# Kernel optimization log

Measured on AMD Instinct MI355X. Metric: run time of the kernel, lower is better.

## Reference

```python
import jax, jax.numpy as jnp
import numpy as np
from functools import partial

H = 51  # hidden size hard-coded in the module


def _lstm_cell(x, h, c, W_ih, b_ih, W_hh, b_hh):
    # PyTorch LSTMCell gate order: i, f, g, o stacked along dim 0 of W (4H rows)
    gates = x @ W_ih.T + b_ih + h @ W_hh.T + b_hh  # [B, 4H]
    i, f, g, o = jnp.split(gates, 4, axis=-1)
    i = jax.nn.sigmoid(i)
    f = jax.nn.sigmoid(f)
    g = jnp.tanh(g)
    o = jax.nn.sigmoid(o)
    c_new = f * c + i * g
    h_new = o * jnp.tanh(c_new)
    return h_new, c_new


def setup_inputs() -> dict:
    key = jax.random.key(0)
    ks = jax.random.split(key, 11)
    B, T = 2048, 512
    bound = 1.0 / np.sqrt(H)  # torch LSTMCell/Linear default init: U(-1/sqrt(H), 1/sqrt(H))
    u = lambda k, shape: jax.random.uniform(k, shape, jnp.float32, -bound, bound)
    return {
        "x": jax.random.normal(ks[0], (B, T), dtype=jnp.float32),
        "future": 0,
        "W_ih1": u(ks[1], (4 * H, 1)),
        "b_ih1": u(ks[2], (4 * H,)),
        "W_hh1": u(ks[3], (4 * H, H)),
        "b_hh1": u(ks[4], (4 * H,)),
        "W_ih2": u(ks[5], (4 * H, H)),
        "b_ih2": u(ks[6], (4 * H,)),
        "W_hh2": u(ks[7], (4 * H, H)),
        "b_hh2": u(ks[8], (4 * H,)),
        "fc_w": u(ks[9], (1, H)),
        "fc_b": u(ks[10], (1,)),
    }


def reference(x, future, W_ih1, b_ih1, W_hh1, b_hh1,
              W_ih2, b_ih2, W_hh2, b_hh2, fc_w, fc_b):
    B = x.shape[0]
    z = jnp.zeros((B, H), dtype=x.dtype)

    def cell_stack(x_t, carry):
        h1, c1, h2, c2 = carry
        h1, c1 = _lstm_cell(x_t, h1, c1, W_ih1, b_ih1, W_hh1, b_hh1)
        h2, c2 = _lstm_cell(h1, h2, c2, W_ih2, b_ih2, W_hh2, b_hh2)
        out = h2 @ fc_w.T + fc_b  # [B, 1]
        return (h1, c1, h2, c2), out

    def step(carry, x_t):
        return cell_stack(x_t, carry)

    xs = jnp.swapaxes(x, 0, 1)[:, :, None]  # [T, B, 1]
    carry, outs = jax.lax.scan(step, (z, z, z, z), xs)  # outs: [T, B, 1]
    outputs = jnp.swapaxes(outs[:, :, 0], 0, 1)  # [B, T]

    if future > 0:
        last = outs[-1]  # [B, 1]

        def fstep(c, _):
            inner, out = c
            inner, out = cell_stack(out, inner)
            return (inner, out), out

        _, fouts = jax.lax.scan(fstep, (carry, last), None, length=future)
        outputs = jnp.concatenate([outputs, jnp.swapaxes(fouts[:, :, 0], 0, 1)], axis=1)

    return outputs
```

## Files before the change

### kernel.cpp

```cpp
#include <hip/hip_runtime.h>

#define HID   51
#define T_LEN 512
#define BT    8
#define NTH   832

#define X_OFF   0
#define OUT_OFF 4128
#define H1_OFF  8256
#define H2_OFF  9280

typedef _Float16 h8 __attribute__((ext_vector_type(8)));
typedef float    f4 __attribute__((ext_vector_type(4)));

__device__ __forceinline__ float fast_rcp(float x) { return __builtin_amdgcn_rcpf(x); }
__device__ __forceinline__ float sigm(float x) { return fast_rcp(1.0f + __expf(-x)); }
__device__ __forceinline__ float tanh_f(float x) {
    x = fminf(15.0f, fmaxf(-15.0f, x));
    float e = __expf(2.0f * x);
    return (e - 1.0f) * fast_rcp(e + 1.0f);
}
__device__ __forceinline__ float tanh_nc(float x) {
    float e = __expf(2.0f * x);
    return (e - 1.0f) * fast_rcp(e + 1.0f);
}

__device__ __forceinline__ float dpp_ror8(float v) {
    int t = __builtin_amdgcn_update_dpp(0, __float_as_int(v), 0x128, 0xf, 0xf, true);
    return __int_as_float(t);
}

__device__ __forceinline__ h8 cvt_frag1(const float* p) {
    float4 a = *(const float4*)p;
    float4 b = *(const float4*)(p + 4);
    h8 h;
    h[0] = (_Float16)a.x; h[1] = (_Float16)a.y; h[2] = (_Float16)a.z; h[3] = (_Float16)a.w;
    h[4] = (_Float16)b.x; h[5] = (_Float16)b.y; h[6] = (_Float16)b.z; h[7] = (_Float16)b.w;
    return h;
}

__device__ __forceinline__ float gate_update(const float G[4], float& c) {
    float iv = sigm(G[0]), fv = sigm(G[1]), gv = tanh_nc(G[2]), ov = sigm(G[3]);
    c = fv * c + iv * gv;
    return ov * tanh_f(c);
}

#define MFMA16(A, B, C) __builtin_amdgcn_mfma_f32_16x16x32_f16((A), (B), (C), 0, 0, 0)

__global__ __launch_bounds__(NTH)
void lstm_seq_kernel(const float* __restrict__ x,
                     const float* __restrict__ W_ih1, const float* __restrict__ b_ih1,
                     const float* __restrict__ W_hh1, const float* __restrict__ b_hh1,
                     const float* __restrict__ W_ih2, const float* __restrict__ b_ih2,
                     const float* __restrict__ W_hh2, const float* __restrict__ b_hh2,
                     const float* __restrict__ fc_w,  const float* __restrict__ fc_b,
                     float* __restrict__ out)
{
    __shared__ __align__(16) float sb[13312];

    const int tid   = threadIdx.x;
    const int b0    = blockIdx.x * BT;
    const int w     = tid >> 6;
    const int lane  = tid & 63;
    const int row16 = lane & 15;
    const int q4    = lane >> 4;
    const int col   = row16;

    h8 a1f[2];
    h8 a2f[4];

    for (int i = tid; i < 208 * 64; i += NTH) {
        int rp = i >> 6, k = i & 63;
        int j = rp >> 2, g = rp & 3;
        float v = 0.0f;
        if (j < HID) {
            if (k < HID)       v = W_hh1[(g * HID + j) * HID + k];
            else if (k == HID) v = W_ih1[g * HID + j];
        }
        sb[i] = v;
    }
    __syncthreads();
    #pragma unroll
    for (int kt = 0; kt < 2; ++kt)
        a1f[kt] = cvt_frag1(sb + (w * 16 + row16) * 64 + kt * 32 + q4 * 8);
    __syncthreads();

    for (int i = tid; i < 208 * 64; i += NTH) {
        int rp = i >> 6, k = i & 63;
        int j = rp >> 2, g = rp & 3;
        sb[i] = (j < HID && k < HID) ? W_ih2[(g * HID + j) * HID + k] : 0.0f;
    }
    __syncthreads();
    #pragma unroll
    for (int kt = 0; kt < 2; ++kt)
        a2f[kt] = cvt_frag1(sb + (w * 16 + row16) * 64 + kt * 32 + q4 * 8);
    __syncthreads();

    for (int i = tid; i < 208 * 64; i += NTH) {
        int rp = i >> 6, k = i & 63;
        int j = rp >> 2, g = rp & 3;
        float v = 0.0f;
        if (k < HID) {
            if (j < HID)        v = W_hh2[(g * HID + j) * HID + k];
            else if (rp == 204) v = fc_w[k];
        }
        sb[i] = v;
    }
    __syncthreads();
    #pragma unroll
    for (int kt = 0; kt < 2; ++kt)
        a2f[kt + 2] = cvt_frag1(sb + (w * 16 + row16) * 64 + kt * 32 + q4 * 8);
    __syncthreads();

    const int jq = 4 * w + q4;
    f4 bi1, bi2;
    #pragma unroll
    for (int g = 0; g < 4; ++g) {
        bi1[g] = (jq < HID) ? (b_ih1[g * HID + jq] + b_hh1[g * HID + jq]) : 0.f;
        bi2[g] = (jq < HID) ? (b_ih2[g * HID + jq] + b_hh2[g * HID + jq]) : 0.f;
    }
    const bool lay1 = (col < 8);
    const int  bsel = col & 7;
    const bool val  = (jq < HID);
    const int offh  = (lay1 ? H1_OFF : H2_OFF) * 2
                    + (jq >> 5) * 512 + ((((jq & 31) >> 3) << 4) + bsel) * 8 + (jq & 7);
    const bool xw = (jq == HID) && lay1;

    float* xl   = sb + X_OFF;
    float* outl = sb + OUT_OFF;
    for (int i = tid; i < BT * 516; i += NTH) {
        int b = i / 516, t = i - 516 * b;
        xl[i] = (t < T_LEN) ? x[(size_t)(b0 + b) * T_LEN + t] : 0.0f;
    }
    for (int i = tid; i < 2048; i += NTH) sb[H1_OFF + i] = 0.0f;

    float c = 0.f;
    const float fcb = fc_b[0];
    const bool outlane = (w == 12) && (q4 == 3) && (col < 8);
    const float* xq  = xl + bsel * 516;
    const float* rA0 = sb + H1_OFF + lane * 4;
    const float* rB0 = sb + H2_OFF + lane * 4;
    _Float16* hwp = (_Float16*)sb + offh;
    __syncthreads();

    if (lay1) {
        if (val) {
            float xv = xq[0];
            float G[4];
            #pragma unroll
            for (int g = 0; g < 4; ++g)
                G[g] = bi1[g] + W_ih1[g * HID + jq] * xv;
            float hv = gate_update(G, c);
            hwp[0] = (_Float16)hv;
        } else if (xw) {
            hwp[0] = (_Float16)xq[1];
        }
    }
    __syncthreads();

    auto body = [&](int i, int p) {
        const float* rA = rA0 + p * 512;
        const float* rB = rB0 + p * 512;
        h8 bh0 = *(const h8*)(rA);       h8 bh1 = *(const h8*)(rA + 256);
        h8 ch2 = *(const h8*)(rB);       h8 ch3 = *(const h8*)(rB + 256);

        if (xw) hwp[(p ^ 1) * 1024] = (_Float16)xq[i + 2];

        f4 s = bi1;
        s = MFMA16(a1f[0], bh0, s);
        s = MFMA16(a1f[1], bh1, s);
        f4 u = bi2;
        u = MFMA16(a2f[0], bh0, u);
        u = MFMA16(a2f[1], bh1, u);
        u = MFMA16(a2f[2], ch2, u);
        u = MFMA16(a2f[3], ch3, u);

        float fcv = u[0];
        float G[4];
        #pragma unroll
        for (int g = 0; g < 4; ++g) {
            float ur = dpp_ror8(u[g]);
            G[g] = lay1 ? s[g] : ur;
        }
        float hv = gate_update(G, c);
        if (val) hwp[(p ^ 1) * 1024] = (_Float16)hv;
        if (outlane && i >= 1) outl[col * 516 + (i - 1)] = fcb + fcv;
        __syncthreads();
    };
    for (int i = 0; i < T_LEN; i += 2) {
        body(i, 0);
        body(i + 1, 1);
    }
    body(T_LEN, 0);

    for (int i = tid; i < BT * T_LEN; i += NTH) {
        int b = i >> 9, tt = i & (T_LEN - 1);
        out[(size_t)(b0 + b) * T_LEN + tt] = outl[b * 516 + tt];
    }
}

extern "C" void kernel_launch(void* const* d_in, const int* in_sizes, int n_in,
                              void* d_out, int out_size, void* d_ws, size_t ws_size,
                              hipStream_t stream) {
    const float* x      = (const float*)d_in[0];
    const float* W_ih1  = (const float*)d_in[2];
    const float* b_ih1v = (const float*)d_in[3];
    const float* W_hh1  = (const float*)d_in[4];
    const float* b_hh1v = (const float*)d_in[5];
    const float* W_ih2  = (const float*)d_in[6];
    const float* b_ih2v = (const float*)d_in[7];
    const float* W_hh2  = (const float*)d_in[8];
    const float* b_hh2v = (const float*)d_in[9];
    const float* fc_w   = (const float*)d_in[10];
    const float* fc_b   = (const float*)d_in[11];
    float* out = (float*)d_out;

    dim3 grid(2048 / BT);
    dim3 block(NTH);
    lstm_seq_kernel<<<grid, block, 0, stream>>>(x, W_ih1, b_ih1v, W_hh1, b_hh1v,
                                                W_ih2, b_ih2v, W_hh2, b_hh2v,
                                                fc_w, fc_b, out);
}
```

Measured before the change: 376.6 us.

## Fold log2e scaling and biases into weights and split MFMA accumulation chain

Gate weights are pre-scaled by log2(e), or 2*log2(e) for the tanh gate, so the activations can call exp2 directly. Bias sums move into an extra weight column that multiplies a constant fp16 1.0 written into the hidden-state buffer, which removes the per-step bias accumulator setup. The second-layer MFMA chain is split into two independent accumulations that are summed at the end, shortening the serial dependency on each recurrent step. The trade-offs are that biases are now rounded to fp16 and the tanh clamp is gone, relying on the rcp formulation staying stable at extreme inputs.

```diff
diff --git a/kernel.cpp b/kernel.cpp
--- a/kernel.cpp
+++ b/kernel.cpp
@@ -10,19 +10,22 @@
 #define H1_OFF  8256
 #define H2_OFF  9280
 
+#define L2E 1.4426950408889634f
+
 typedef _Float16 h8 __attribute__((ext_vector_type(8)));
 typedef float    f4 __attribute__((ext_vector_type(4)));
 
 __device__ __forceinline__ float fast_rcp(float x) { return __builtin_amdgcn_rcpf(x); }
-__device__ __forceinline__ float sigm(float x) { return fast_rcp(1.0f + __expf(-x)); }
-__device__ __forceinline__ float tanh_f(float x) {
-    x = fminf(15.0f, fmaxf(-15.0f, x));
-    float e = __expf(2.0f * x);
-    return (e - 1.0f) * fast_rcp(e + 1.0f);
-}
-__device__ __forceinline__ float tanh_nc(float x) {
-    float e = __expf(2.0f * x);
-    return (e - 1.0f) * fast_rcp(e + 1.0f);
+
+#if __has_builtin(__builtin_amdgcn_exp2f)
+__device__ __forceinline__ float exp2_f(float x) { return __builtin_amdgcn_exp2f(x); }
+#else
+__device__ __forceinline__ float exp2_f(float x) { return exp2f(x); }
+#endif
+
+__device__ __forceinline__ float sigm2(float X) { return fast_rcp(1.0f + exp2_f(-X)); }
+__device__ __forceinline__ float tanh2(float E) {
+    return fmaf(-2.0f, fast_rcp(exp2_f(E) + 1.0f), 1.0f);
 }
 
 __device__ __forceinline__ float dpp_ror8(float v) {
@@ -40,9 +43,12 @@
 }
 
 __device__ __forceinline__ float gate_update(const float G[4], float& c) {
-    float iv = sigm(G[0]), fv = sigm(G[1]), gv = tanh_nc(G[2]), ov = sigm(G[3]);
-    c = fv * c + iv * gv;
-    return ov * tanh_f(c);
+    float iv = sigm2(G[0]);
+    float fv = sigm2(G[1]);
+    float gv = tanh2(G[2]);
+    float ov = sigm2(G[3]);
+    c = fmaf(fv, c, iv * gv);
+    return ov * tanh2(c * (2.0f * L2E));
 }
 
 #define MFMA16(A, B, C) __builtin_amdgcn_mfma_f32_16x16x32_f16((A), (B), (C), 0, 0, 0)
@@ -72,10 +78,12 @@
     for (int i = tid; i < 208 * 64; i += NTH) {
         int rp = i >> 6, k = i & 63;
         int j = rp >> 2, g = rp & 3;
+        float sc = (g == 2) ? 2.0f * L2E : L2E;
         float v = 0.0f;
         if (j < HID) {
-            if (k < HID)       v = W_hh1[(g * HID + j) * HID + k];
-            else if (k == HID) v = W_ih1[g * HID + j];
+            if (k < HID)           v = W_hh1[(g * HID + j) * HID + k] * sc;
+            else if (k == HID)     v = W_ih1[g * HID + j] * sc;
+            else if (k == HID + 1) v = (b_ih1[g * HID + j] + b_hh1[g * HID + j]) * sc;
         }
         sb[i] = v;
     }
@@ -88,7 +96,13 @@
     for (int i = tid; i < 208 * 64; i += NTH) {
         int rp = i >> 6, k = i & 63;
         int j = rp >> 2, g = rp & 3;
-        sb[i] = (j < HID && k < HID) ? W_ih2[(g * HID + j) * HID + k] : 0.0f;
+        float sc = (g == 2) ? 2.0f * L2E : L2E;
+        float v = 0.0f;
+        if (j < HID) {
+            if (k < HID)           v = W_ih2[(g * HID + j) * HID + k] * sc;
+            else if (k == HID + 1) v = (b_ih2[g * HID + j] + b_hh2[g * HID + j]) * sc;
+        }
+        sb[i] = v;
     }
     __syncthreads();
     #pragma unroll
@@ -99,9 +113,10 @@
     for (int i = tid; i < 208 * 64; i += NTH) {
         int rp = i >> 6, k = i & 63;
         int j = rp >> 2, g = rp & 3;
+        float sc = (g == 2) ? 2.0f * L2E : L2E;
         float v = 0.0f;
         if (k < HID) {
-            if (j < HID)        v = W_hh2[(g * HID + j) * HID + k];
+            if (j < HID)        v = W_hh2[(g * HID + j) * HID + k] * sc;
             else if (rp == 204) v = fc_w[k];
         }
         sb[i] = v;
@@ -113,12 +128,6 @@
     __syncthreads();
 
     const int jq = 4 * w + q4;
-    f4 bi1, bi2;
-    #pragma unroll
-    for (int g = 0; g < 4; ++g) {
-        bi1[g] = (jq < HID) ? (b_ih1[g * HID + jq] + b_hh1[g * HID + jq]) : 0.f;
-        bi2[g] = (jq < HID) ? (b_ih2[g * HID + jq] + b_hh2[g * HID + jq]) : 0.f;
-    }
     const bool lay1 = (col < 8);
     const int  bsel = col & 7;
     const bool val  = (jq < HID);
@@ -132,7 +141,15 @@
         int b = i / 516, t = i - 516 * b;
         xl[i] = (t < T_LEN) ? x[(size_t)(b0 + b) * T_LEN + t] : 0.0f;
     }
-    for (int i = tid; i < 2048; i += NTH) sb[H1_OFF + i] = 0.0f;
+    for (int i = tid; i < 2048; i += NTH) {
+        int w32 = 0;
+        if (i < 1024) {
+            int r = i & 511;
+            int d = r - 386;
+            if (d >= 0 && d < 32 && (d & 3) == 0) w32 = 0x00003C00;
+        }
+        ((int*)(sb + H1_OFF))[i] = w32;
+    }
 
     float c = 0.f;
     const float fcb = fc_b[0];
@@ -141,6 +158,7 @@
     const float* rA0 = sb + H1_OFF + lane * 4;
     const float* rB0 = sb + H2_OFF + lane * 4;
     _Float16* hwp = (_Float16*)sb + offh;
+    const f4 z4 = {0.f, 0.f, 0.f, 0.f};
     __syncthreads();
 
     if (lay1) {
@@ -148,8 +166,11 @@
             float xv = xq[0];
             float G[4];
             #pragma unroll
-            for (int g = 0; g < 4; ++g)
-                G[g] = bi1[g] + W_ih1[g * HID + jq] * xv;
+            for (int g = 0; g < 4; ++g) {
+                float sc = (g == 2) ? 2.0f * L2E : L2E;
+                float bs = b_ih1[g * HID + jq] + b_hh1[g * HID + jq];
+                G[g] = sc * fmaf(W_ih1[g * HID + jq], xv, bs);
+            }
             float hv = gate_update(G, c);
             hwp[0] = (_Float16)hv;
         } else if (xw) {
@@ -166,14 +187,13 @@
 
         if (xw) hwp[(p ^ 1) * 1024] = (_Float16)xq[i + 2];
 
-        f4 s = bi1;
-        s = MFMA16(a1f[0], bh0, s);
-        s = MFMA16(a1f[1], bh1, s);
-        f4 u = bi2;
-        u = MFMA16(a2f[0], bh0, u);
-        u = MFMA16(a2f[1], bh1, u);
-        u = MFMA16(a2f[2], ch2, u);
-        u = MFMA16(a2f[3], ch3, u);
+        f4 s   = MFMA16(a1f[0], bh0, z4);
+        s      = MFMA16(a1f[1], bh1, s);
+        f4 u01 = MFMA16(a2f[0], bh0, z4);
+        u01    = MFMA16(a2f[1], bh1, u01);
+        f4 u23 = MFMA16(a2f[2], ch2, z4);
+        u23    = MFMA16(a2f[3], ch3, u23);
+        f4 u   = u01 + u23;
 
         float fcv = u[0];
         float G[4];
```

Result: no change. 377.3 us (+0.2%).
